# Kernel optimization log

Measured on AMD Instinct MI355X. Metric: run time of the kernel, lower is better.

The kernel has to match this reference:

```python
import jax, jax.numpy as jnp
import numpy as np
from jax import lax


def conv2d(x, w, b=None, pad=1):
    y = lax.conv_general_dilated(x, w, (1, 1), [(pad, pad), (pad, pad)],
                                 dimension_numbers=('NCHW', 'OIHW', 'NCHW'))
    return y if b is None else y + b[None, :, None, None]


def conv3d(x, w, b=None, pad=(0, 0, 0), dil=(1, 1, 1), groups=1):
    y = lax.conv_general_dilated(x, w, (1, 1, 1), [(p, p) for p in pad],
                                 rhs_dilation=dil,
                                 dimension_numbers=('NCDHW', 'OIDHW', 'NCDHW'),
                                 feature_group_count=groups)
    return y if b is None else y + b[None, :, None, None, None]


def base_grid(H, W, dtype):
    # normalized grid, channel 0 = x in [-1,1], channel 1 = y in [-1,1]
    gxn = 2.0 * jnp.arange(W, dtype=dtype) / max(W - 1, 1) - 1.0
    gyn = 2.0 * jnp.arange(H, dtype=dtype) / max(H - 1, 1) - 1.0
    return jnp.stack([jnp.broadcast_to(gxn[None, :], (H, W)),
                      jnp.broadcast_to(gyn[:, None], (H, W))], 0)


def grid_sample(img, grid):
    # img (N,C,H,W), grid (N,H,W,2) in [-1,1] (x,y); bilinear, zeros padding, align_corners=False
    N, C, H, W = img.shape
    gx = ((grid[..., 0] + 1.0) * W - 1.0) * 0.5
    gy = ((grid[..., 1] + 1.0) * H - 1.0) * 0.5
    x0 = jnp.floor(gx)
    y0 = jnp.floor(gy)
    wx = gx - x0
    wy = gy - y0

    def one(im, x0b, y0b, wxb, wyb):
        x0i = x0b.astype(jnp.int32)
        y0i = y0b.astype(jnp.int32)

        def samp(xi, yi):
            valid = (xi >= 0) & (xi < W) & (yi >= 0) & (yi < H)
            v = im[:, jnp.clip(yi, 0, H - 1), jnp.clip(xi, 0, W - 1)]
            return v * valid[None].astype(im.dtype)

        v00 = samp(x0i, y0i)
        v01 = samp(x0i + 1, y0i)
        v10 = samp(x0i, y0i + 1)
        v11 = samp(x0i + 1, y0i + 1)
        return (v00 * (1 - wxb) * (1 - wyb) + v01 * wxb * (1 - wyb)
                + v10 * (1 - wxb) * wyb + v11 * wxb * wyb)

    return jax.vmap(one)(img, x0, y0, wx, wy)


def ms_def_corr(x, y, off):
    # deformable correlation: per scale, warp y by that scale's offset and take
    # the channel-mean dot product with x -> (BT, S, H, W)
    BT, C, H, W = x.shape
    base = base_grid(H, W, x.dtype)
    sc = jnp.array([W - 1, H - 1], x.dtype)[None, :, None, None]
    S = off.shape[1] // 2
    corrs = []
    for i in range(S):
        vg = base[None] + off[:, 2 * i:2 * i + 2] / sc
        w = grid_sample(y, vg.transpose(0, 2, 3, 1))
        corrs.append(jnp.mean(x * w, axis=1))
    return jnp.stack(corrs, 1)


def corr_filter(corr, w1, w2):
    avg = jnp.mean(corr, 1, keepdims=True)
    mx = jnp.max(corr, 1, keepdims=True)
    var = jnp.var(corr, axis=1, keepdims=True, ddof=1)  # torch.var unbiased
    attn = jax.nn.sigmoid(conv2d(jnp.concatenate([avg, mx], 1), w1) + conv2d(var, w2))
    return corr * attn


def setup_inputs() -> dict:
    key = jax.random.key(0)
    ks = jax.random.split(key, 16)
    B, C, T, H, W = 2, 64, 16, 64, 64
    S = 3
    r = C // 16

    def n(k, shape, s=0.02):
        return jax.random.normal(k, shape, jnp.float32) * s

    return {
        'x': jax.random.normal(ks[0], (B, C, T, H, W), jnp.float32),
        'ofs_l_w1': n(ks[1], (C, 2 * C, 3, 3)), 'ofs_l_b1': jnp.zeros((C,), jnp.float32),
        'ofs_l_w2': n(ks[2], (2 * S, C, 3, 3)), 'ofs_l_b2': jnp.zeros((2 * S,), jnp.float32),
        'ofs_r_w1': n(ks[3], (C, 2 * C, 3, 3)), 'ofs_r_b1': jnp.zeros((C,), jnp.float32),
        'ofs_r_w2': n(ks[4], (2 * S, C, 3, 3)), 'ofs_r_b2': jnp.zeros((2 * S,), jnp.float32),
        'cf_w1': n(ks[5], (1, 2, 3, 3), 0.1), 'cf_w2': n(ks[6], (1, 1, 3, 3), 0.1),
        'down_w': n(ks[7], (r, C, 1, 1, 1), 0.1),
        'sa1_w': n(ks[8], (r, 1, 9, 3, 3), 0.1), 'sa1_b': jnp.zeros((r,), jnp.float32),
        'sa2_w': n(ks[9], (r, 1, 9, 3, 3), 0.1), 'sa2_b': jnp.zeros((r,), jnp.float32),
        'sa3_w': n(ks[10], (r, 1, 9, 3, 3), 0.1), 'sa3_b': jnp.zeros((r,), jnp.float32),
        'agg_w': jnp.ones((3,), jnp.float32) / 3,
        'back_w': n(ks[11], (C, r, 1, 1, 1), 0.1),
        'fusion_w': jnp.ones((2,), jnp.float32) / 2,
    }


def reference(x, ofs_l_w1, ofs_l_b1, ofs_l_w2, ofs_l_b2,
              ofs_r_w1, ofs_r_b1, ofs_r_w2, ofs_r_b2,
              cf_w1, cf_w2, down_w,
              sa1_w, sa1_b, sa2_w, sa2_b, sa3_w, sa3_b,
              agg_w, back_w, fusion_w):
    B, C, T, H, W = x.shape
    r = down_w.shape[0]

    # long-term branch: 1x1x1 down conv -> 3 dilated depthwise 3D convs -> 1x1x1 up conv
    x_agg = conv3d(x, down_w)
    agg = (conv3d(x_agg, sa1_w, sa1_b, (4, 1, 1), (1, 1, 1), r) * agg_w[0]
           + conv3d(x_agg, sa2_w, sa2_b, (4, 2, 2), (1, 2, 2), r) * agg_w[1]
           + conv3d(x_agg, sa3_w, sa3_b, (4, 3, 3), (1, 3, 3), r) * agg_w[2])
    long_term = jax.nn.sigmoid(conv3d(agg, back_w)) - 0.5

    # temporal shifts
    left = jnp.concatenate([x[:, :, 1:], x[:, :, -1:]], 2)
    right = jnp.concatenate([x[:, :, :1], x[:, :, :-1]], 2)
    xf = x.transpose(0, 2, 1, 3, 4).reshape(B * T, C, H, W)
    lf = left.transpose(0, 2, 1, 3, 4).reshape(B * T, C, H, W)
    rf = right.transpose(0, 2, 1, 3, 4).reshape(B * T, C, H, W)

    off_lm = conv2d(jax.nn.relu(conv2d(jnp.concatenate([xf, lf], 1), ofs_l_w1, ofs_l_b1)),
                    ofs_l_w2, ofs_l_b2)
    off_rm = conv2d(jax.nn.relu(conv2d(jnp.concatenate([xf, rf], 1), ofs_r_w1, ofs_r_b1)),
                    ofs_r_w2, ofs_r_b2)

    corr_lm = ms_def_corr(xf, lf, off_lm)
    corr_rm = ms_def_corr(xf, rf, off_rm)
    fcl = corr_filter(corr_lm, cf_w1, cf_w2)
    fcr = corr_filter(corr_rm, cf_w1, cf_w2)

    base = base_grid(H, W, x.dtype)
    sc = jnp.array([W - 1, H - 1], x.dtype)[None, :, None, None]
    vg_lm = base[None] + off_lm[:, :2] / sc
    vg_rm = base[None] + off_rm[:, :2] / sc
    warped_lm = grid_sample(lf, vg_lm.transpose(0, 2, 3, 1))
    warped_rm = grid_sample(rf, vg_rm.transpose(0, 2, 3, 1))

    attn_lm = jnp.mean(fcl, 1, keepdims=True)
    attn_rm = jnp.mean(fcr, 1, keepdims=True)
    feat_lm = warped_lm * (jax.nn.sigmoid(attn_lm) - 0.5)
    feat_rm = warped_rm * (jax.nn.sigmoid(attn_rm) - 0.5)

    short = fusion_w[0] * feat_lm + fusion_w[1] * feat_rm
    short = short.reshape(B, T, C, H, W).transpose(0, 2, 1, 3, 4)
    return short * long_term
```

## Files before the change

kernel.cpp:

```cpp
#include <hip/hip_runtime.h>
#include <hip/hip_bf16.h>
#include <math.h>


typedef __attribute__((ext_vector_type(8))) short short8v;
typedef __attribute__((ext_vector_type(4))) float f32x4;

__device__ __forceinline__ float sigmoidf_(float v) {
    return 1.0f / (1.0f + expf(-v));
}

__device__ __forceinline__ float bf2f(short s) {
    union { unsigned u; float f; } z;
    z.u = ((unsigned)(unsigned short)s) << 16;
    return z.f;
}

__device__ __forceinline__ void gll16(const __hip_bfloat16* g, __hip_bfloat16* l) {
    __builtin_amdgcn_global_load_lds((const __attribute__((address_space(1))) unsigned int*)(const void*)g,
                                     (__attribute__((address_space(3))) unsigned int*)(void*)l,
                                     16, 0, 0);
}

struct Samp { int o0, o1, o2, o3; float w0, w1, w2, w3; };

__device__ __forceinline__ Samp make_samp(float ox, float oy, int w, int h) {
    float bx = (2.0f * (float)w) / 63.0f - 1.0f;
    float by = (2.0f * (float)h) / 63.0f - 1.0f;
    float vx = bx + ox / 63.0f;
    float vy = by + oy / 63.0f;
    float gx = ((vx + 1.0f) * 64.0f - 1.0f) * 0.5f;
    float gy = ((vy + 1.0f) * 64.0f - 1.0f) * 0.5f;
    float fx = floorf(gx), fy = floorf(gy);
    float wx = gx - fx, wy = gy - fy;
    int x0 = (int)fx, y0 = (int)fy;
    int x1 = x0 + 1, y1 = y0 + 1;
    bool vx0 = (x0 >= 0) && (x0 < 64), vx1 = (x1 >= 0) && (x1 < 64);
    bool vy0 = (y0 >= 0) && (y0 < 64), vy1 = (y1 >= 0) && (y1 < 64);
    int cx0 = min(max(x0, 0), 63), cx1 = min(max(x1, 0), 63);
    int cy0 = min(max(y0, 0), 63), cy1 = min(max(y1, 0), 63);
    Samp s;
    s.o0 = cy0 * 4224 + (cx0 + 1) * 64; s.w0 = (1.0f - wx) * (1.0f - wy) * ((vx0 && vy0) ? 1.0f : 0.0f);
    s.o1 = cy0 * 4224 + (cx1 + 1) * 64; s.w1 = wx * (1.0f - wy) * ((vx1 && vy0) ? 1.0f : 0.0f);
    s.o2 = cy1 * 4224 + (cx0 + 1) * 64; s.w2 = (1.0f - wx) * wy * ((vx0 && vy1) ? 1.0f : 0.0f);
    s.o3 = cy1 * 4224 + (cx1 + 1) * 64; s.w3 = wx * wy * ((vx1 && vy1) ? 1.0f : 0.0f);
    return s;
}

__global__ __launch_bounds__(256) void k_prep_x(const float* __restrict__ x,
                                                __hip_bfloat16* __restrict__ xT)
{
    int bid = blockIdx.x;
    int h = bid & 63;
    int n = bid >> 6;
    int b = n >> 4, t = n & 15;
    __shared__ float s[64][65];
    int tid = threadIdx.x;
    for (int idx = tid; idx < 4096; idx += 256) {
        int c = idx >> 6, w = idx & 63;
        s[c][w] = x[(((size_t)b * 64 + c) * 16 + t) * 4096 + h * 64 + w];
    }
    __syncthreads();
    __hip_bfloat16* op = xT + ((size_t)n * 64 + h) * 4224;
    for (int idx = tid; idx < 4224; idx += 256) {
        int wp = idx >> 6, c = idx & 63;
        float v = (wp == 0 || wp == 65) ? 0.f : s[c][wp - 1];
        op[idx] = __float2bfloat16(v);
    }
}

__global__ __launch_bounds__(256) void k_prep_w(const float* __restrict__ wl1,
                                                const float* __restrict__ wr1,
                                                const float* __restrict__ wl2,
                                                const float* __restrict__ wr2,
                                                __hip_bfloat16* __restrict__ Wmisc,
                                                __hip_bfloat16* __restrict__ hidden)
{
    int idx = blockIdx.x * 256 + threadIdx.x;
    if (idx < 147456) {
        int side = (idx >= 73728) ? 1 : 0;
        int i = idx - side * 73728;
        int ci = i & 127;
        int co = (i >> 7) & 63;
        int tap = i >> 13;
        const float* w = side ? wr1 : wl1;
        float v = w[((size_t)co * 128 + ci) * 9 + tap];
        int pos = side * 73728 + tap * 8192 + co * 128 + (ci ^ ((co & 15) << 3));
        Wmisc[pos] = __float2bfloat16(v);
    } else if (idx < 151680) {
        Wmisc[idx] = __float2bfloat16(0.f);
    } else if (idx < 170112) {
        int i2 = idx - 151680;
        int side = i2 / 9216;
        int j = i2 - side * 9216;
        int tap = j >> 10;
        int rem = j & 1023;
        int co = rem >> 6;
        int ci = rem & 63;
        const float* w = side ? wr2 : wl2;
        float v = (co < 6) ? w[((size_t)co * 64 + ci) * 9 + tap] : 0.f;
        Wmisc[idx] = __float2bfloat16(v);
    } else if (idx < 432256) {
        int i3 = idx - 170112;
        int co = i3 & 63;
        int sel = (i3 >> 6) & 1;
        int rr = (i3 >> 7) & 63;
        int nn = i3 >> 13;
        hidden[((size_t)(nn * 64 + rr) * 66 + (sel ? 65 : 0)) * 64 + co] = __float2bfloat16(0.f);
    }
}

__global__ __launch_bounds__(256) void k_conv1_mfma(const __hip_bfloat16* __restrict__ xT,
                                                    const __hip_bfloat16* __restrict__ Wb,
                                                    const __hip_bfloat16* __restrict__ zrow,
                                                    const float* __restrict__ b1,
                                                    __hip_bfloat16* __restrict__ hidden,
                                                    int dir)
{
    __shared__ __hip_bfloat16 sB[2][8192];

    int bid = blockIdx.x;
    int rp = bid & 31;
    int n = bid >> 5;
    int b = n >> 4, t = n & 15;
    int t2 = (dir > 0) ? min(t + 1, 15) : max(t - 1, 0);
    int n2 = b * 16 + t2;

    int tid = threadIdx.x;
    int wv = tid >> 6;
    int lane = tid & 63;
    int r = rp * 2 + (wv & 1);
    int m0 = (wv >> 1) * 32;
    int lr = lane & 15;
    int q = lane >> 4;
    int lk = q << 3;

    const __hip_bfloat16* fA0 = xT + (size_t)n * 270336;
    const __hip_bfloat16* fA1 = xT + (size_t)n2 * 270336;

    f32x4 acc[2][4];
    #pragma unroll
    for (int ni = 0; ni < 4; ni++) {
        float bb = b1[ni * 16 + lr];
        acc[0][ni] = (f32x4){bb, bb, bb, bb};
        acc[1][ni] = (f32x4){bb, bb, bb, bb};
    }

    int kx[2][2];
    #pragma unroll
    for (int khalf = 0; khalf < 2; khalf++)
        #pragma unroll
        for (int ks = 0; ks < 2; ks++)
            kx[khalf][ks] = ((khalf << 7) + (ks << 6) + (q << 4)) ^ (lr << 4);

    #pragma unroll
    for (int i = 0; i < 4; i++)
        gll16(Wb + (size_t)(i * 2048 + wv * 512 + lane * 8), &sB[0][i * 2048 + wv * 512]);
    __syncthreads();

    #pragma unroll
    for (int tap = 0; tap < 9; tap++) {
        const int cur = tap & 1;
        if (tap < 8) {
            const __hip_bfloat16* wsrc = Wb + ((size_t)(tap + 1) << 13);
            #pragma unroll
            for (int i = 0; i < 4; i++)
                gll16(wsrc + (size_t)(i * 2048 + wv * 512 + lane * 8), &sB[cur ^ 1][i * 2048 + wv * 512]);
        }
        const int kh = tap / 3, kw = tap - (tap / 3) * 3;
        int rr = r + kh - 1;
        bool ok = (rr >= 0) && (rr < 64);
        const __hip_bfloat16* r0 = ok ? (fA0 + rr * 4224) : zrow;
        const __hip_bfloat16* r1 = ok ? (fA1 + rr * 4224) : zrow;
        int abase = (m0 + lr + kw) * 64 + lk;
        const char* sbc = (const char*)&sB[cur][0];

        #pragma unroll
        for (int khalf = 0; khalf < 2; khalf++) {
            const __hip_bfloat16* ar = khalf ? r1 : r0;
            short8v a00 = *(const short8v*)(ar + abase);
            short8v a01 = *(const short8v*)(ar + abase + 32);
            short8v a10 = *(const short8v*)(ar + abase + 1024);
            short8v a11 = *(const short8v*)(ar + abase + 1056);
            #pragma unroll
            for (int ni = 0; ni < 4; ni++) {
                int rowb = ni * 4096 + lr * 256;
                short8v b0 = *(const short8v*)(sbc + (rowb + kx[khalf][0]));
                short8v b1v = *(const short8v*)(sbc + (rowb + kx[khalf][1]));
                acc[0][ni] = __builtin_amdgcn_mfma_f32_16x16x32_bf16(a00, b0, acc[0][ni], 0, 0, 0);
                acc[1][ni] = __builtin_amdgcn_mfma_f32_16x16x32_bf16(a10, b0, acc[1][ni], 0, 0, 0);
                acc[0][ni] = __builtin_amdgcn_mfma_f32_16x16x32_bf16(a01, b1v, acc[0][ni], 0, 0, 0);
                acc[1][ni] = __builtin_amdgcn_mfma_f32_16x16x32_bf16(a11, b1v, acc[1][ni], 0, 0, 0);
            }
        }
        __syncthreads();
    }

    int pxq = q << 2;
    __hip_bfloat16* hb = hidden + (size_t)(n * 64 + r) * 66 * 64;
    #pragma unroll
    for (int mi = 0; mi < 2; mi++) {
        #pragma unroll
        for (int ni = 0; ni < 4; ni++) {
            int co = ni * 16 + lr;
            #pragma unroll
            for (int j = 0; j < 4; j++) {
                int px = m0 + mi * 16 + pxq + j;
                float v = acc[mi][ni][j];
                v = v < 0.f ? 0.f : v;
                hb[(size_t)(px + 1) * 64 + co] = __float2bfloat16(v);
            }
        }
    }
}

__global__ __launch_bounds__(256) void k_conv2_mfma(const __hip_bfloat16* __restrict__ hidden,
                                                    const __hip_bfloat16* __restrict__ W2b,
                                                    const __hip_bfloat16* __restrict__ zrow,
                                                    const float* __restrict__ b2,
                                                    float* __restrict__ off)
{
    int bid = blockIdx.x;
    int rq = bid & 15;
    int n = bid >> 4;
    int tid = threadIdx.x;
    int wv = tid >> 6;
    int lane = tid & 63;
    int r = rq * 4 + wv;
    int lr = lane & 15;
    int lk = (lane >> 4) << 3;

    const __hip_bfloat16* hbase = hidden + (size_t)n * 270336;

    float bb = (lr < 6) ? b2[lr] : 0.f;
    f32x4 acc[4];
    #pragma unroll
    for (int mi = 0; mi < 4; mi++) acc[mi] = (f32x4){bb, bb, bb, bb};

    #pragma unroll
    for (int tap = 0; tap < 9; tap++) {
        const int kh = tap / 3, kw = tap - (tap / 3) * 3;
        int rr = r + kh - 1;
        bool ok = (rr >= 0) && (rr < 64);
        const __hip_bfloat16* hr = ok ? (hbase + (size_t)rr * 4224) : zrow;
        const __hip_bfloat16* bw = W2b + ((size_t)tap * 16 + lr) * 64 + lk;
        short8v b0 = *(const short8v*)(bw);
        short8v b1v = *(const short8v*)(bw + 32);
        #pragma unroll
        for (int mi = 0; mi < 4; mi++) {
            int abase = (mi * 16 + lr + kw) * 64 + lk;
            short8v a0 = *(const short8v*)(hr + abase);
            short8v a1 = *(const short8v*)(hr + abase + 32);
            acc[mi] = __builtin_amdgcn_mfma_f32_16x16x32_bf16(a0, b0, acc[mi], 0, 0, 0);
            acc[mi] = __builtin_amdgcn_mfma_f32_16x16x32_bf16(a1, b1v, acc[mi], 0, 0, 0);
        }
    }
    if (lr < 6) {
        int pxq = (lane >> 4) << 2;
        #pragma unroll
        for (int mi = 0; mi < 4; mi++) {
            #pragma unroll
            for (int j = 0; j < 4; j++) {
                int px = mi * 16 + pxq + j;
                off[((size_t)n * 6 + lr) * 4096 + r * 64 + px] = acc[mi][j];
            }
        }
    }
}

__global__ __launch_bounds__(256) void k_down(const float* __restrict__ x,
                                              const float* __restrict__ dw,
                                              float* __restrict__ xa)
{
    int gid = blockIdx.x * 256 + threadIdx.x;
    int hw = gid & 4095;
    int bt = gid >> 12;
    int b = bt >> 4, t = bt & 15;
    float a0 = 0.f, a1 = 0.f, a2 = 0.f, a3 = 0.f;
    const float* xp = x + (((size_t)b * 64) * 16 + t) * 4096 + hw;
    for (int c = 0; c < 64; c++) {
        float v = xp[(size_t)c * 65536];
        a0 = fmaf(v, dw[c], a0);
        a1 = fmaf(v, dw[64 + c], a1);
        a2 = fmaf(v, dw[128 + c], a2);
        a3 = fmaf(v, dw[192 + c], a3);
    }
    size_t base = (((size_t)b * 4) * 16 + t) * 4096 + hw;
    xa[base] = a0;
    xa[base + 65536] = a1;
    xa[base + 131072] = a2;
    xa[base + 196608] = a3;
}

__global__ __launch_bounds__(256) void k_agg(const float* __restrict__ xa,
                                             const float* __restrict__ w1, const float* __restrict__ b1,
                                             const float* __restrict__ w2, const float* __restrict__ b2,
                                             const float* __restrict__ w3, const float* __restrict__ b3,
                                             const float* __restrict__ aw,
                                             float* __restrict__ agg)
{
    int gid = blockIdx.x * 256 + threadIdx.x;
    int hw = gid & 4095;
    int rest = gid >> 12;
    int t = rest & 15;
    int g = (rest >> 4) & 3;
    int b = rest >> 6;
    int h = hw >> 6, w = hw & 63;
    const float* base = xa + ((size_t)(b * 4 + g) * 16) * 4096;
    const float* ws0 = w1 + g * 81;
    const float* ws1 = w2 + g * 81;
    const float* ws2 = w3 + g * 81;
    float acc0 = b1[g], acc1 = b2[g], acc2 = b3[g];
    for (int kd = 0; kd < 9; kd++) {
        int d = t + kd - 4;
        if (d < 0 || d > 15) continue;
        const float* fr = base + (size_t)d * 4096;
        #pragma unroll
        for (int kh = 0; kh < 3; kh++) {
            #pragma unroll
            for (int kw = 0; kw < 3; kw++) {
                int widx = kd * 9 + kh * 3 + kw;
                {
                    int yy = h + (kh - 1), xx = w + (kw - 1);
                    if (yy >= 0 && yy < 64 && xx >= 0 && xx < 64)
                        acc0 = fmaf(fr[yy * 64 + xx], ws0[widx], acc0);
                }
                {
                    int yy = h + (kh - 1) * 2, xx = w + (kw - 1) * 2;
                    if (yy >= 0 && yy < 64 && xx >= 0 && xx < 64)
                        acc1 = fmaf(fr[yy * 64 + xx], ws1[widx], acc1);
                }
                {
                    int yy = h + (kh - 1) * 3, xx = w + (kw - 1) * 3;
                    if (yy >= 0 && yy < 64 && xx >= 0 && xx < 64)
                        acc2 = fmaf(fr[yy * 64 + xx], ws2[widx], acc2);
                }
            }
        }
    }
    agg[gid] = acc0 * aw[0] + acc1 * aw[1] + acc2 * aw[2];
}

__global__ __launch_bounds__(256) void k_corr(const __hip_bfloat16* __restrict__ xT,
                                              const float* __restrict__ off,
                                              float* __restrict__ stats, int dir)
{
    int gid = blockIdx.x * 256 + threadIdx.x;
    int hw = gid & 4095;
    int n = gid >> 12;
    int b = n >> 4, t = n & 15;
    int t2 = (dir > 0) ? min(t + 1, 15) : max(t - 1, 0);
    int n2 = b * 16 + t2;
    int h = hw >> 6, w = hw & 63;

    const __hip_bfloat16* xf = xT + (size_t)n * 270336 + h * 4224 + (w + 1) * 64;
    const __hip_bfloat16* yf = xT + (size_t)n2 * 270336;

    Samp sp[3];
    #pragma unroll
    for (int s = 0; s < 3; s++) {
        float ox = off[((size_t)n * 6 + 2 * s) * 4096 + hw];
        float oy = off[((size_t)n * 6 + 2 * s + 1) * 4096 + hw];
        sp[s] = make_samp(ox, oy, w, h);
    }

    float ac[3][4];
    #pragma unroll
    for (int s = 0; s < 3; s++)
        #pragma unroll
        for (int qq = 0; qq < 4; qq++) ac[s][qq] = 0.f;

    for (int cc = 0; cc < 64; cc += 8) {
        short8v xv = *(const short8v*)(xf + cc);
        #pragma unroll
        for (int s = 0; s < 3; s++) {
            short8v v0 = *(const short8v*)(yf + sp[s].o0 + cc);
            short8v v1 = *(const short8v*)(yf + sp[s].o1 + cc);
            short8v v2 = *(const short8v*)(yf + sp[s].o2 + cc);
            short8v v3 = *(const short8v*)(yf + sp[s].o3 + cc);
            #pragma unroll
            for (int e = 0; e < 8; e++) {
                float xe = bf2f(xv[e]);
                ac[s][0] = fmaf(xe, bf2f(v0[e]), ac[s][0]);
                ac[s][1] = fmaf(xe, bf2f(v1[e]), ac[s][1]);
                ac[s][2] = fmaf(xe, bf2f(v2[e]), ac[s][2]);
                ac[s][3] = fmaf(xe, bf2f(v3[e]), ac[s][3]);
            }
        }
    }
    float c[3];
    #pragma unroll
    for (int s = 0; s < 3; s++)
        c[s] = (ac[s][0] * sp[s].w0 + ac[s][1] * sp[s].w1 + ac[s][2] * sp[s].w2 + ac[s][3] * sp[s].w3) * (1.0f / 64.0f);
    float avg = (c[0] + c[1] + c[2]) * (1.0f / 3.0f);
    float mx = fmaxf(c[0], fmaxf(c[1], c[2]));
    float d0 = c[0] - avg, d1 = c[1] - avg, d2 = c[2] - avg;
    float var = (d0 * d0 + d1 * d1 + d2 * d2) * 0.5f;
    stats[(size_t)n * 4096 + hw] = avg;
    stats[131072 + (size_t)n * 4096 + hw] = mx;
    stats[262144 + (size_t)n * 4096 + hw] = var;
}

__device__ __forceinline__ float attn_val(const float* __restrict__ stats, int n, int hw,
                                          const float* __restrict__ cfw1,
                                          const float* __restrict__ cfw2)
{
    int h = hw >> 6, w = hw & 63;
    const float* avg = stats + (size_t)n * 4096;
    const float* mx  = stats + 131072 + (size_t)n * 4096;
    const float* var = stats + 262144 + (size_t)n * 4096;
    float s = 0.f;
    #pragma unroll
    for (int k = 0; k < 9; k++) {
        int kh = k / 3 - 1, kw = k - (k / 3) * 3 - 1;
        int yy = h + kh, xx = w + kw;
        if (yy >= 0 && yy < 64 && xx >= 0 && xx < 64) {
            int p = yy * 64 + xx;
            s += avg[p] * cfw1[k] + mx[p] * cfw1[9 + k] + var[p] * cfw2[k];
        }
    }
    float attn = sigmoidf_(s);
    return sigmoidf_(avg[hw] * attn) - 0.5f;
}

__global__ __launch_bounds__(256) void k_final(const __hip_bfloat16* __restrict__ xT,
                                               const float* __restrict__ off_l,
                                               const float* __restrict__ off_r,
                                               const float* __restrict__ stats_l,
                                               const float* __restrict__ stats_r,
                                               const float* __restrict__ cfw1,
                                               const float* __restrict__ cfw2,
                                               const float* __restrict__ agg,
                                               const float* __restrict__ backw,
                                               const float* __restrict__ fusw,
                                               float* __restrict__ out)
{
    int gid = blockIdx.x * 256 + threadIdx.x;
    int hw = gid & 4095;
    int n = gid >> 12;
    int b = n >> 4, t = n & 15;
    int tl = min(t + 1, 15), tr = max(t - 1, 0);
    int nl = b * 16 + tl, nr = b * 16 + tr;
    int h = hw >> 6, w = hw & 63;

    float oxl = off_l[((size_t)n * 6 + 0) * 4096 + hw];
    float oyl = off_l[((size_t)n * 6 + 1) * 4096 + hw];
    float oxr = off_r[((size_t)n * 6 + 0) * 4096 + hw];
    float oyr = off_r[((size_t)n * 6 + 1) * 4096 + hw];
    Samp sl = make_samp(oxl, oyl, w, h);
    Samp sr = make_samp(oxr, oyr, w, h);

    const __hip_bfloat16* lf = xT + (size_t)nl * 270336;
    const __hip_bfloat16* rf = xT + (size_t)nr * 270336;

    float Al = attn_val(stats_l, n, hw, cfw1, cfw2) * fusw[0];
    float Ar = attn_val(stats_r, n, hw, cfw1, cfw2) * fusw[1];

    float ag0 = agg[((size_t)(b * 4 + 0) * 16 + t) * 4096 + hw];
    float ag1 = agg[((size_t)(b * 4 + 1) * 16 + t) * 4096 + hw];
    float ag2 = agg[((size_t)(b * 4 + 2) * 16 + t) * 4096 + hw];
    float ag3 = agg[((size_t)(b * 4 + 3) * 16 + t) * 4096 + hw];

    for (int cc = 0; cc < 64; cc += 8) {
        short8v l0 = *(const short8v*)(lf + sl.o0 + cc);
        short8v l1 = *(const short8v*)(lf + sl.o1 + cc);
        short8v l2 = *(const short8v*)(lf + sl.o2 + cc);
        short8v l3 = *(const short8v*)(lf + sl.o3 + cc);
        short8v r0 = *(const short8v*)(rf + sr.o0 + cc);
        short8v r1 = *(const short8v*)(rf + sr.o1 + cc);
        short8v r2 = *(const short8v*)(rf + sr.o2 + cc);
        short8v r3 = *(const short8v*)(rf + sr.o3 + cc);
        #pragma unroll
        for (int e = 0; e < 8; e++) {
            int c = cc + e;
            float wl = sl.w0 * bf2f(l0[e]) + sl.w1 * bf2f(l1[e]) + sl.w2 * bf2f(l2[e]) + sl.w3 * bf2f(l3[e]);
            float wr = sr.w0 * bf2f(r0[e]) + sr.w1 * bf2f(r1[e]) + sr.w2 * bf2f(r2[e]) + sr.w3 * bf2f(r3[e]);
            float lt = sigmoidf_(ag0 * backw[c * 4 + 0] + ag1 * backw[c * 4 + 1]
                               + ag2 * backw[c * 4 + 2] + ag3 * backw[c * 4 + 3]) - 0.5f;
            out[(((size_t)b * 64 + c) * 16 + t) * 4096 + hw] = (wl * Al + wr * Ar) * lt;
        }
    }
}

extern "C" void kernel_launch(void* const* d_in, const int* in_sizes, int n_in,
                              void* d_out, int out_size, void* d_ws, size_t ws_size,
                              hipStream_t stream)
{
    const float* x     = (const float*)d_in[0];
    const float* lw1   = (const float*)d_in[1];
    const float* lb1   = (const float*)d_in[2];
    const float* lw2   = (const float*)d_in[3];
    const float* lb2   = (const float*)d_in[4];
    const float* rw1   = (const float*)d_in[5];
    const float* rb1   = (const float*)d_in[6];
    const float* rw2   = (const float*)d_in[7];
    const float* rb2   = (const float*)d_in[8];
    const float* cfw1  = (const float*)d_in[9];
    const float* cfw2  = (const float*)d_in[10];
    const float* downw = (const float*)d_in[11];
    const float* sa1w  = (const float*)d_in[12];
    const float* sa1b  = (const float*)d_in[13];
    const float* sa2w  = (const float*)d_in[14];
    const float* sa2b  = (const float*)d_in[15];
    const float* sa3w  = (const float*)d_in[16];
    const float* sa3b  = (const float*)d_in[17];
    const float* aggw  = (const float*)d_in[18];
    const float* backw = (const float*)d_in[19];
    const float* fusw  = (const float*)d_in[20];
    float* out = (float*)d_out;

    float* ws      = (float*)d_ws;
    float* x_agg   = ws;
    float* agg     = x_agg + 524288;
    float* off_l   = agg + 524288;
    float* off_r   = off_l + 786432;
    float* stats_l = off_r + 786432;
    float* stats_r = stats_l + 393216;
    __hip_bfloat16* hidden = (__hip_bfloat16*)(stats_r + 393216);
    __hip_bfloat16* xT     = hidden + 8650752;
    __hip_bfloat16* Wmisc  = xT + 8650752;
    __hip_bfloat16* Wb     = Wmisc;
    __hip_bfloat16* zrow   = Wmisc + 147456;
    __hip_bfloat16* W2bL   = Wmisc + 151680;
    __hip_bfloat16* W2bR   = W2bL + 9216;

    k_prep_x<<<2048, 256, 0, stream>>>(x, xT);
    k_prep_w<<<1689, 256, 0, stream>>>(lw1, rw1, lw2, rw2, Wmisc, hidden);

    k_down<<<512, 256, 0, stream>>>(x, downw, x_agg);
    k_agg<<<2048, 256, 0, stream>>>(x_agg, sa1w, sa1b, sa2w, sa2b, sa3w, sa3b, aggw, agg);

    k_conv1_mfma<<<1024, 256, 0, stream>>>(xT, Wb, zrow, lb1, hidden, +1);
    k_conv2_mfma<<<512, 256, 0, stream>>>(hidden, W2bL, zrow, lb2, off_l);
    k_corr<<<512, 256, 0, stream>>>(xT, off_l, stats_l, +1);

    k_conv1_mfma<<<1024, 256, 0, stream>>>(xT, Wb + 73728, zrow, rb1, hidden, -1);
    k_conv2_mfma<<<512, 256, 0, stream>>>(hidden, W2bR, zrow, rb2, off_r);
    k_corr<<<512, 256, 0, stream>>>(xT, off_r, stats_r, -1);

    k_final<<<512, 256, 0, stream>>>(xT, off_l, off_r, stats_l, stats_r, cfw1, cfw2,
                                     agg, backw, fusw, out);
}
```

Before: 302.0 us.

## Fuse channel downsample into prep, batch temporal agg, restructure conv1 tiling

Folds the 1x1 channel-reduction kernel into the x transpose kernel, computing it from the shared-memory tile already loaded there. This removes a separate pass over x and one launch. The temporal aggregation kernel now computes four time steps per thread so each loaded input value feeds several outputs. conv1 moves to 512-thread blocks covering four rows, and loads weights for three taps at a time with fewer barriers instead of double-buffering one tap at a time. In exchange there is more shared memory per block, weight loads are no longer overlapped with MFMA work, and agg now launches fewer threads.

Result: slower. 337.2 us (+11.7%).

```diff
diff --git a/kernel.cpp b/kernel.cpp
--- a/kernel.cpp
+++ b/kernel.cpp
@@ -48,7 +48,9 @@
 }
 
 __global__ __launch_bounds__(256) void k_prep_x(const float* __restrict__ x,
-                                                __hip_bfloat16* __restrict__ xT)
+                                                const float* __restrict__ dw,
+                                                __hip_bfloat16* __restrict__ xT,
+                                                float* __restrict__ xa)
 {
     int bid = blockIdx.x;
     int h = bid & 63;
@@ -67,6 +69,12 @@
         float v = (wp == 0 || wp == 65) ? 0.f : s[c][wp - 1];
         op[idx] = __float2bfloat16(v);
     }
+    int w = tid & 63, g = tid >> 6;
+    float acc = 0.f;
+    const float* dwg = dw + g * 64;
+    #pragma unroll 8
+    for (int c = 0; c < 64; c++) acc = fmaf(s[c][w], dwg[c], acc);
+    xa[((size_t)(b * 4 + g) * 16 + t) * 4096 + h * 64 + w] = acc;
 }
 
 __global__ __launch_bounds__(256) void k_prep_w(const float* __restrict__ wl1,
@@ -110,18 +118,18 @@
     }
 }
 
-__global__ __launch_bounds__(256) void k_conv1_mfma(const __hip_bfloat16* __restrict__ xT,
-                                                    const __hip_bfloat16* __restrict__ Wb,
-                                                    const __hip_bfloat16* __restrict__ zrow,
-                                                    const float* __restrict__ b1,
-                                                    __hip_bfloat16* __restrict__ hidden,
-                                                    int dir)
-{
-    __shared__ __hip_bfloat16 sB[2][8192];
+__global__ __launch_bounds__(512, 4) void k_conv1_mfma(const __hip_bfloat16* __restrict__ xT,
+                                                       const __hip_bfloat16* __restrict__ Wb,
+                                                       const __hip_bfloat16* __restrict__ zrow,
+                                                       const float* __restrict__ b1,
+                                                       __hip_bfloat16* __restrict__ hidden,
+                                                       int dir)
+{
+    __shared__ __hip_bfloat16 sB[24576];
 
     int bid = blockIdx.x;
-    int rp = bid & 31;
-    int n = bid >> 5;
+    int rq = bid & 15;
+    int n = bid >> 4;
     int b = n >> 4, t = n & 15;
     int t2 = (dir > 0) ? min(t + 1, 15) : max(t - 1, 0);
     int n2 = b * 16 + t2;
@@ -129,8 +137,8 @@
     int tid = threadIdx.x;
     int wv = tid >> 6;
     int lane = tid & 63;
-    int r = rp * 2 + (wv & 1);
-    int m0 = (wv >> 1) * 32;
+    int r = rq * 4 + (wv & 3);
+    int m0 = (wv >> 2) * 32;
     int lr = lane & 15;
     int q = lane >> 4;
     int lk = q << 3;
@@ -153,47 +161,46 @@
         for (int ks = 0; ks < 2; ks++)
             kx[khalf][ks] = ((khalf << 7) + (ks << 6) + (q << 4)) ^ (lr << 4);
 
-    #pragma unroll
-    for (int i = 0; i < 4; i++)
-        gll16(Wb + (size_t)(i * 2048 + wv * 512 + lane * 8), &sB[0][i * 2048 + wv * 512]);
-    __syncthreads();
-
-    #pragma unroll
-    for (int tap = 0; tap < 9; tap++) {
-        const int cur = tap & 1;
-        if (tap < 8) {
-            const __hip_bfloat16* wsrc = Wb + ((size_t)(tap + 1) << 13);
+    const char* sbc = (const char*)&sB[0];
+
+    #pragma unroll
+    for (int g = 0; g < 3; g++) {
+        __syncthreads();
+        {
+            const __hip_bfloat16* wsrc = Wb + (size_t)g * 24576 + wv * 3072 + lane * 8;
             #pragma unroll
-            for (int i = 0; i < 4; i++)
-                gll16(wsrc + (size_t)(i * 2048 + wv * 512 + lane * 8), &sB[cur ^ 1][i * 2048 + wv * 512]);
-        }
-        const int kh = tap / 3, kw = tap - (tap / 3) * 3;
-        int rr = r + kh - 1;
+            for (int j = 0; j < 6; j++)
+                gll16(wsrc + j * 512, &sB[wv * 3072 + j * 512]);
+        }
+        __syncthreads();
+
+        int rr = r + g - 1;
         bool ok = (rr >= 0) && (rr < 64);
         const __hip_bfloat16* r0 = ok ? (fA0 + rr * 4224) : zrow;
         const __hip_bfloat16* r1 = ok ? (fA1 + rr * 4224) : zrow;
-        int abase = (m0 + lr + kw) * 64 + lk;
-        const char* sbc = (const char*)&sB[cur][0];
-
-        #pragma unroll
-        for (int khalf = 0; khalf < 2; khalf++) {
-            const __hip_bfloat16* ar = khalf ? r1 : r0;
-            short8v a00 = *(const short8v*)(ar + abase);
-            short8v a01 = *(const short8v*)(ar + abase + 32);
-            short8v a10 = *(const short8v*)(ar + abase + 1024);
-            short8v a11 = *(const short8v*)(ar + abase + 1056);
+
+        #pragma unroll
+        for (int tl = 0; tl < 3; tl++) {
+            int abase = (m0 + lr + tl) * 64 + lk;
             #pragma unroll
-            for (int ni = 0; ni < 4; ni++) {
-                int rowb = ni * 4096 + lr * 256;
-                short8v b0 = *(const short8v*)(sbc + (rowb + kx[khalf][0]));
-                short8v b1v = *(const short8v*)(sbc + (rowb + kx[khalf][1]));
-                acc[0][ni] = __builtin_amdgcn_mfma_f32_16x16x32_bf16(a00, b0, acc[0][ni], 0, 0, 0);
-                acc[1][ni] = __builtin_amdgcn_mfma_f32_16x16x32_bf16(a10, b0, acc[1][ni], 0, 0, 0);
-                acc[0][ni] = __builtin_amdgcn_mfma_f32_16x16x32_bf16(a01, b1v, acc[0][ni], 0, 0, 0);
-                acc[1][ni] = __builtin_amdgcn_mfma_f32_16x16x32_bf16(a11, b1v, acc[1][ni], 0, 0, 0);
+            for (int khalf = 0; khalf < 2; khalf++) {
+                const __hip_bfloat16* ar = khalf ? r1 : r0;
+                short8v a00 = *(const short8v*)(ar + abase);
+                short8v a01 = *(const short8v*)(ar + abase + 32);
+                short8v a10 = *(const short8v*)(ar + abase + 1024);
+                short8v a11 = *(const short8v*)(ar + abase + 1056);
+                #pragma unroll
+                for (int ni = 0; ni < 4; ni++) {
+                    int rowb = tl * 16384 + ni * 4096 + lr * 256;
+                    short8v b0  = *(const short8v*)(sbc + (rowb + kx[khalf][0]));
+                    short8v b1v = *(const short8v*)(sbc + (rowb + kx[khalf][1]));
+                    acc[0][ni] = __builtin_amdgcn_mfma_f32_16x16x32_bf16(a00, b0, acc[0][ni], 0, 0, 0);
+                    acc[1][ni] = __builtin_amdgcn_mfma_f32_16x16x32_bf16(a10, b0, acc[1][ni], 0, 0, 0);
+                    acc[0][ni] = __builtin_amdgcn_mfma_f32_16x16x32_bf16(a01, b1v, acc[0][ni], 0, 0, 0);
+                    acc[1][ni] = __builtin_amdgcn_mfma_f32_16x16x32_bf16(a11, b1v, acc[1][ni], 0, 0, 0);
+                }
             }
         }
-        __syncthreads();
     }
 
     int pxq = q << 2;
@@ -268,30 +275,6 @@
     }
 }
 
-__global__ __launch_bounds__(256) void k_down(const float* __restrict__ x,
-                                              const float* __restrict__ dw,
-                                              float* __restrict__ xa)
-{
-    int gid = blockIdx.x * 256 + threadIdx.x;
-    int hw = gid & 4095;
-    int bt = gid >> 12;
-    int b = bt >> 4, t = bt & 15;
-    float a0 = 0.f, a1 = 0.f, a2 = 0.f, a3 = 0.f;
-    const float* xp = x + (((size_t)b * 64) * 16 + t) * 4096 + hw;
-    for (int c = 0; c < 64; c++) {
-        float v = xp[(size_t)c * 65536];
-        a0 = fmaf(v, dw[c], a0);
-        a1 = fmaf(v, dw[64 + c], a1);
-        a2 = fmaf(v, dw[128 + c], a2);
-        a3 = fmaf(v, dw[192 + c], a3);
-    }
-    size_t base = (((size_t)b * 4) * 16 + t) * 4096 + hw;
-    xa[base] = a0;
-    xa[base + 65536] = a1;
-    xa[base + 131072] = a2;
-    xa[base + 196608] = a3;
-}
-
 __global__ __launch_bounds__(256) void k_agg(const float* __restrict__ xa,
                                              const float* __restrict__ w1, const float* __restrict__ b1,
                                              const float* __restrict__ w2, const float* __restrict__ b2,
@@ -302,43 +285,53 @@
     int gid = blockIdx.x * 256 + threadIdx.x;
     int hw = gid & 4095;
     int rest = gid >> 12;
-    int t = rest & 15;
-    int g = (rest >> 4) & 3;
-    int b = rest >> 6;
+    int tq = rest & 3;
+    int g = (rest >> 2) & 3;
+    int b = rest >> 4;
+    int t0 = tq * 4;
     int h = hw >> 6, w = hw & 63;
+
     const float* base = xa + ((size_t)(b * 4 + g) * 16) * 4096;
     const float* ws0 = w1 + g * 81;
     const float* ws1 = w2 + g * 81;
     const float* ws2 = w3 + g * 81;
-    float acc0 = b1[g], acc1 = b2[g], acc2 = b3[g];
-    for (int kd = 0; kd < 9; kd++) {
-        int d = t + kd - 4;
-        if (d < 0 || d > 15) continue;
-        const float* fr = base + (size_t)d * 4096;
-        #pragma unroll
-        for (int kh = 0; kh < 3; kh++) {
+
+    float acc0[4], acc1[4], acc2[4];
+    #pragma unroll
+    for (int ti = 0; ti < 4; ti++) { acc0[ti] = b1[g]; acc1[ti] = b2[g]; acc2[ti] = b3[g]; }
+
+    int d0 = max(0, t0 - 4), d1 = min(15, t0 + 7);
+
+    #pragma unroll
+    for (int kh = 0; kh < 3; kh++) {
+        #pragma unroll
+        for (int kw = 0; kw < 3; kw++) {
+            int tap = kh * 3 + kw;
             #pragma unroll
-            for (int kw = 0; kw < 3; kw++) {
-                int widx = kd * 9 + kh * 3 + kw;
-                {
-                    int yy = h + (kh - 1), xx = w + (kw - 1);
-                    if (yy >= 0 && yy < 64 && xx >= 0 && xx < 64)
-                        acc0 = fmaf(fr[yy * 64 + xx], ws0[widx], acc0);
-                }
-                {
-                    int yy = h + (kh - 1) * 2, xx = w + (kw - 1) * 2;
-                    if (yy >= 0 && yy < 64 && xx >= 0 && xx < 64)
-                        acc1 = fmaf(fr[yy * 64 + xx], ws1[widx], acc1);
-                }
-                {
-                    int yy = h + (kh - 1) * 3, xx = w + (kw - 1) * 3;
-                    if (yy >= 0 && yy < 64 && xx >= 0 && xx < 64)
-                        acc2 = fmaf(fr[yy * 64 + xx], ws2[widx], acc2);
+            for (int s = 0; s < 3; s++) {
+                int dil = s + 1;
+                int yy = h + (kh - 1) * dil, xx = w + (kw - 1) * dil;
+                if (yy < 0 || yy > 63 || xx < 0 || xx > 63) continue;
+                const float* wsS = (s == 0) ? ws0 : (s == 1) ? ws1 : ws2;
+                float* accS = (s == 0) ? acc0 : (s == 1) ? acc1 : acc2;
+                const float* col = base + yy * 64 + xx;
+                for (int d = d0; d <= d1; d++) {
+                    float val = col[(size_t)d * 4096];
+                    #pragma unroll
+                    for (int ti = 0; ti < 4; ti++) {
+                        int kd = d - t0 - ti + 4;
+                        if (kd >= 0 && kd <= 8)
+                            accS[ti] = fmaf(val, wsS[kd * 9 + tap], accS[ti]);
+                    }
                 }
             }
         }
     }
-    agg[gid] = acc0 * aw[0] + acc1 * aw[1] + acc2 * aw[2];
+    #pragma unroll
+    for (int ti = 0; ti < 4; ti++) {
+        agg[((size_t)(b * 4 + g) * 16 + t0 + ti) * 4096 + hw] =
+            acc0[ti] * aw[0] + acc1[ti] * aw[1] + acc2[ti] * aw[2];
+    }
 }
 
 __global__ __launch_bounds__(256) void k_corr(const __hip_bfloat16* __restrict__ xT,
@@ -524,17 +517,16 @@
     __hip_bfloat16* W2bL   = Wmisc + 151680;
     __hip_bfloat16* W2bR   = W2bL + 9216;
 
-    k_prep_x<<<2048, 256, 0, stream>>>(x, xT);
+    k_prep_x<<<2048, 256, 0, stream>>>(x, downw, xT, x_agg);
     k_prep_w<<<1689, 256, 0, stream>>>(lw1, rw1, lw2, rw2, Wmisc, hidden);
 
-    k_down<<<512, 256, 0, stream>>>(x, downw, x_agg);
-    k_agg<<<2048, 256, 0, stream>>>(x_agg, sa1w, sa1b, sa2w, sa2b, sa3w, sa3b, aggw, agg);
-
-    k_conv1_mfma<<<1024, 256, 0, stream>>>(xT, Wb, zrow, lb1, hidden, +1);
+    k_agg<<<512, 256, 0, stream>>>(x_agg, sa1w, sa1b, sa2w, sa2b, sa3w, sa3b, aggw, agg);
+
+    k_conv1_mfma<<<512, 512, 0, stream>>>(xT, Wb, zrow, lb1, hidden, +1);
     k_conv2_mfma<<<512, 256, 0, stream>>>(hidden, W2bL, zrow, lb2, off_l);
     k_corr<<<512, 256, 0, stream>>>(xT, off_l, stats_l, +1);
 
-    k_conv1_mfma<<<1024, 256, 0, stream>>>(xT, Wb + 73728, zrow, rb1, hidden, -1);
+    k_conv1_mfma<<<512, 512, 0, stream>>>(xT, Wb + 73728, zrow, rb1, hidden, -1);
     k_conv2_mfma<<<512, 256, 0, stream>>>(hidden, W2bR, zrow, rb2, off_r);
     k_corr<<<512, 256, 0, stream>>>(xT, off_r, stats_r, -1);
 
```
